# Kernel tuning notes

Measured on AMD Instinct MI355X. Metric: run time of the kernel, lower is better.

## Reference

```python
import jax, jax.numpy as jnp
import numpy as np

B, T, C, H, D, E, K = 4, 1024, 1024, 16, 64, 8, 2
HID = 2 * D  # expert MLP hidden width (assumed 2*head_dim)
NEG = jnp.finfo(jnp.float32).min


def setup_inputs() -> dict:
    key = jax.random.key(0)
    ks = jax.random.split(key, 16)
    s = 0.02
    # rotary tables [max_pos, head_dim]
    inv_freq = 1.0 / (10000.0 ** (jnp.arange(0, D, 2, dtype=jnp.float32) / D))
    freqs = jnp.arange(T, dtype=jnp.float32)[:, None] * inv_freq[None, :]
    emb = jnp.concatenate([freqs, freqs], axis=-1)  # [T, D]
    return {
        "x": jax.random.normal(ks[0], (B, T, C), jnp.float32),
        "position_ids": jnp.sort(jax.random.randint(ks[1], (B, T), 0, T), axis=-1),
        "cos": jnp.cos(emb),
        "sin": jnp.sin(emb),
        "rq": s * jax.random.normal(ks[2], (D, E), jnp.float32),
        "rk": s * jax.random.normal(ks[3], (D, E), jnp.float32),
        "rv": s * jax.random.normal(ks[4], (D, E), jnp.float32),
        "q_w1": s * jax.random.normal(ks[5], (E, D, HID), jnp.float32),
        "q_w2": s * jax.random.normal(ks[6], (E, HID, D), jnp.float32),
        "k_w1": s * jax.random.normal(ks[7], (E, D, HID), jnp.float32),
        "k_w2": s * jax.random.normal(ks[8], (E, HID, D), jnp.float32),
        "v_w1": s * jax.random.normal(ks[9], (E, D, HID), jnp.float32),
        "v_w2": s * jax.random.normal(ks[10], (E, HID, D), jnp.float32),
        "o_w": s * jax.random.normal(ks[11], (C, C), jnp.float32),  # torch Linear weight [out,in]
    }


def _rotate_half(x):
    x1, x2 = x[..., : D // 2], x[..., D // 2:]
    return jnp.concatenate([-x2, x1], axis=-1)


def _moe_head_proj(xh, r_w, w1, w2):
    """Per-head top-k routed expert MLP. xh: [B,T,H,D]."""
    logits = jnp.einsum('bthd,de->bthe', xh, r_w)            # router logits
    vals, idx = jax.lax.top_k(logits, K)                     # [B,T,H,K]
    w = jax.nn.softmax(vals, axis=-1)
    onehot = jax.nn.one_hot(idx, E, dtype=xh.dtype)          # [B,T,H,K,E]
    w_full = jnp.einsum('bthk,bthke->bthe', w, onehot)       # scatter weights to all experts
    h = jax.nn.gelu(jnp.einsum('bthd,edf->bthef', xh, w1))   # all-expert hidden
    out = jnp.einsum('bthe,bthef,efg->bthg', w_full, h, w2)  # masked weighted combine
    return out, logits


def reference(x, position_ids, cos, sin, rq, rk, rv, q_w1, q_w2, k_w1, k_w2, v_w1, v_w2, o_w):
    xh = x.reshape(B, T, H, D)
    q, _ = _moe_head_proj(xh, rq, q_w1, q_w2)
    k, _ = _moe_head_proj(xh, rk, k_w1, k_w2)
    v, _ = _moe_head_proj(xh, rv, v_w1, v_w2)
    q = q.transpose(0, 2, 1, 3)  # [B,H,T,D]
    k = k.transpose(0, 2, 1, 3)
    v = v.transpose(0, 2, 1, 3)
    # RoPE
    c = cos[position_ids][:, None, :, :]  # [B,1,T,D]
    s = sin[position_ids][:, None, :, :]
    q = q * c + _rotate_half(q) * s
    k = k * c + _rotate_half(k) * s
    # causal SDPA
    scores = jnp.einsum('bhqd,bhkd->bhqk', q, k) / jnp.sqrt(jnp.float32(D))
    causal = jnp.tril(jnp.ones((T, T), dtype=bool))
    scores = jnp.where(causal, scores, NEG)
    attn = jax.nn.softmax(scores, axis=-1)
    out = jnp.einsum('bhqk,bhkd->bhqd', attn, v)
    out = out.transpose(0, 2, 1, 3).reshape(B, T, C)
    return out @ o_w.T
```

## Files before the change

### kernel.cpp

```cpp
#include <hip/hip_runtime.h>
#include <math.h>

#define BB 4
#define TT 1024
#define CCH 1024
#define HH 16
#define DD 64
#define EE 8
#define HID 128
#define CAP 8192
#define GEXP 504

typedef unsigned short u16;
typedef unsigned int u32;
typedef short bf16x8 __attribute__((ext_vector_type(8)));
typedef float f32x4 __attribute__((ext_vector_type(4)));

__device__ __forceinline__ u16 f2bf(float f) {
    unsigned int u = __float_as_uint(f);
    unsigned int r = (u + 0x7FFFu + ((u >> 16) & 1u)) >> 16;
    return (u16)r;
}
__device__ __forceinline__ u16 f2bf_f(float f) {
    return (u16)((__float_as_uint(f) + 0x8000u) >> 16);
}
__device__ __forceinline__ u32 pkbf(float lo, float hi) {
    u32 a = __float_as_uint(lo) + 0x8000u;
    u32 b = __float_as_uint(hi) + 0x8000u;
    return __builtin_amdgcn_perm(b, a, 0x07060302u);
}
__device__ __forceinline__ float gelu_fast(float z) {
    float t = z * z;
    float wn = __builtin_fmaf(t, -0.07135481283f, -1.5957691216f);
    float e = __expf(z * wn);
    return __fdividef(z, 1.f + e);
}

#define GLD16(gp, lp) __builtin_amdgcn_global_load_lds( \
    (const __attribute__((address_space(1))) u32*)(gp), \
    (__attribute__((address_space(3))) u32*)(lp), 16, 0, 0)

__global__ __launch_bounds__(256) void prep_kernel(
    const float* __restrict__ x,
    const float* __restrict__ rq, const float* __restrict__ rk, const float* __restrict__ rv,
    unsigned int* __restrict__ counts,
    unsigned int* __restrict__ idxbuf, float2* __restrict__ wtbuf,
    const float* __restrict__ qw1, const float* __restrict__ kw1, const float* __restrict__ vw1,
    const float* __restrict__ qw2, const float* __restrict__ kw2, const float* __restrict__ vw2,
    u16* __restrict__ img1, u16* __restrict__ img2,
    const float* __restrict__ ow, u16* __restrict__ owbf)
{
    const int bi = blockIdx.x;
    const int tid = threadIdx.x;

    if (bi < 192) {
        int t = bi * 256 + tid;
        u16 tmp[8];
        if (t < 24576) {
            int c = t & 7, f = (t >> 3) & 127, e = (t >> 10) & 7, p = t >> 13;
            const float* w1 = ((p == 0) ? qw1 : (p == 1) ? kw1 : vw1) + e * 8192;
            int dbase = 8 * (c ^ (f & 7));
            #pragma unroll
            for (int j = 0; j < 8; ++j) tmp[j] = f2bf(w1[(dbase + j) * 128 + f]);
            uint4 ov;
            ov.x = (u32)tmp[0] | ((u32)tmp[1] << 16);
            ov.y = (u32)tmp[2] | ((u32)tmp[3] << 16);
            ov.z = (u32)tmp[4] | ((u32)tmp[5] << 16);
            ov.w = (u32)tmp[6] | ((u32)tmp[7] << 16);
            ((uint4*)img1)[t] = ov;
        } else {
            int i = t - 24576;
            int c = i & 15, g = (i >> 4) & 63, e = (i >> 10) & 7, p = i >> 13;
            const float* w2 = ((p == 0) ? qw2 : (p == 1) ? kw2 : vw2) + e * 8192;
            int fbase = 8 * (c ^ (g & 15));
            #pragma unroll
            for (int j = 0; j < 8; ++j) tmp[j] = f2bf(w2[(fbase + j) * 64 + g]);
            uint4 ov;
            ov.x = (u32)tmp[0] | ((u32)tmp[1] << 16);
            ov.y = (u32)tmp[2] | ((u32)tmp[3] << 16);
            ov.z = (u32)tmp[4] | ((u32)tmp[5] << 16);
            ov.w = (u32)tmp[6] | ((u32)tmp[7] << 16);
            ((uint4*)img2)[i] = ov;
        }
        return;
    }

    if (bi < 1216) {
        int i = (bi - 192) * 256 + tid;
        float4 v = ((const float4*)ow)[i];
        unsigned int lov = (unsigned int)f2bf(v.x) | ((unsigned int)f2bf(v.y) << 16);
        unsigned int hiv = (unsigned int)f2bf(v.z) | ((unsigned int)f2bf(v.w) << 16);
        ((uint2*)owbf)[i] = make_uint2(lov, hiv);
        return;
    }

    {
        const unsigned int g = (bi - 1216) * 256 + tid;

        __shared__ float rS[3][64][8];
        __shared__ int lcnt[192];
        __shared__ int lbase[192];

        for (int i = tid; i < 1536; i += 256) {
            int p = i >> 9, rem = i & 511;
            const float* rp = (p == 0) ? rq : (p == 1) ? rk : rv;
            rS[p][rem >> 3][rem & 7] = rp[rem];
        }
        if (tid < 192) lcnt[tid] = 0;
        __syncthreads();

        float lg[3][8];
        #pragma unroll
        for (int p = 0; p < 3; ++p)
            #pragma unroll
            for (int e = 0; e < 8; ++e) lg[p][e] = 0.f;

        const float* xr = x + (size_t)g * 64;
        for (int i4 = 0; i4 < 16; ++i4) {
            float4 xv = ((const float4*)xr)[i4];
            float xa[4] = {xv.x, xv.y, xv.z, xv.w};
            #pragma unroll
            for (int m = 0; m < 4; ++m) {
                int d = i4 * 4 + m;
                #pragma unroll
                for (int p = 0; p < 3; ++p) {
                    float4 r0 = *(const float4*)&rS[p][d][0];
                    float4 r1 = *(const float4*)&rS[p][d][4];
                    lg[p][0] += xa[m] * r0.x; lg[p][1] += xa[m] * r0.y;
                    lg[p][2] += xa[m] * r0.z; lg[p][3] += xa[m] * r0.w;
                    lg[p][4] += xa[m] * r1.x; lg[p][5] += xa[m] * r1.y;
                    lg[p][6] += xa[m] * r1.z; lg[p][7] += xa[m] * r1.w;
                }
            }
        }

        int ppe[3]; float2 pw[3]; int slot[3];
        #pragma unroll
        for (int p = 0; p < 3; ++p) {
            int i1 = 0; float v1 = lg[p][0];
            #pragma unroll
            for (int e = 1; e < 8; ++e) { if (lg[p][e] > v1) { v1 = lg[p][e]; i1 = e; } }
            int i2 = -1; float v2 = -3.402823466e38f;
            #pragma unroll
            for (int e = 0; e < 8; ++e) { if (e != i1 && lg[p][e] > v2) { v2 = lg[p][e]; i2 = e; } }
            float z = __expf(v2 - v1);
            float inv = 1.f / (1.f + z);
            float wa = inv, wb = z * inv;
            int lo = min(i1, i2), hi = max(i1, i2);
            float wlo = (i1 < i2) ? wa : wb;
            float whi = (i1 < i2) ? wb : wa;
            int pel = p * 64 + lo * 8 + hi;
            ppe[p] = pel; pw[p] = make_float2(wlo, whi);
            slot[p] = atomicAdd(&lcnt[pel], 1);
        }
        __syncthreads();
        if (tid < 192) {
            int c = lcnt[tid];
            lbase[tid] = c ? (int)atomicAdd(&counts[tid], (unsigned int)c) : 0;
        }
        __syncthreads();
        #pragma unroll
        for (int p = 0; p < 3; ++p) {
            int pos = lbase[ppe[p]] + slot[p];
            if (pos < CAP) {
                idxbuf[ppe[p] * CAP + pos] = g;
                wtbuf[ppe[p] * CAP + pos]  = pw[p];
            }
        }
    }
}

__global__ __launch_bounds__(128) void sched_kernel(
    const unsigned int* __restrict__ counts, unsigned int* __restrict__ blockinfo)
{
    const int tid = threadIdx.x;
    __shared__ int nsub[84];
    __shared__ int extra[84];
    __shared__ int frac[84];
    __shared__ int alloc[84];
    __shared__ int startS[84];
    __shared__ int nnzS, totalS, rem2S;

    if (tid < 84) {
        int p = tid / 28, q = tid - 28 * p, lo = 0;
        while (q >= 7 - lo) { q -= 7 - lo; ++lo; }
        int hi = lo + 1 + q;
        int n = (int)counts[p * 64 + lo * 8 + hi];
        if (n > CAP) n = CAP;
        nsub[tid] = (n + 31) >> 5;
    }
    __syncthreads();
    if (tid == 0) {
        int tot = 0, nz = 0;
        for (int i = 0; i < 84; ++i) { tot += nsub[i]; nz += (nsub[i] > 0); }
        totalS = tot; nnzS = nz;
    }
    __syncthreads();
    const int R = GEXP - nnzS;
    if (tid < 84) {
        if (nsub[tid] > 0) {
            int e = (int)(((long long)nsub[tid] * R) / totalS);
            extra[tid] = e;
            frac[tid] = nsub[tid] * R - e * totalS;
        } else { extra[tid] = 0; frac[tid] = -1; }
    }
    __syncthreads();
    if (tid == 0) {
        int se = 0;
        for (int i = 0; i < 84; ++i) se += extra[i];
        rem2S = GEXP - nnzS - se;
    }
    __syncthreads();
    if (tid < 84) {
        if (nsub[tid] > 0) {
            int rank = 0;
            for (int j = 0; j < 84; ++j)
                if (nsub[j] > 0 && (frac[j] > frac[tid] || (frac[j] == frac[tid] && j < tid))) ++rank;
            alloc[tid] = 1 + extra[tid] + (rank < rem2S ? 1 : 0);
        } else alloc[tid] = 0;
    }
    __syncthreads();
    if (tid == 0) {
        int s = 0;
        for (int i = 0; i < 84; ++i) { startS[i] = s; s += alloc[i]; }
    }
    __syncthreads();
    if (tid < 84) {
        int a = alloc[tid], st = startS[tid];
        for (int c = 0; c < a; ++c)
            blockinfo[st + c] = (unsigned)tid | ((unsigned)c << 8) | ((unsigned)a << 20);
    }
}

__global__ __launch_bounds__(512, 2) void expert_kernel(
    const float* __restrict__ x, const int* __restrict__ pos_ids,
    const float* __restrict__ cosb, const float* __restrict__ sinb,
    const u16* __restrict__ img1, const u16* __restrict__ img2,
    const unsigned int* __restrict__ counts,
    const unsigned int* __restrict__ idxbuf, const float2* __restrict__ wtbuf,
    const unsigned int* __restrict__ blockinfo,
    u16* __restrict__ qb, u16* __restrict__ kb, u16* __restrict__ vb)
{
    const int tid = threadIdx.x;
    const unsigned int info = blockinfo[blockIdx.x];
    const int pe84 = info & 255;
    const int chunk = (info >> 8) & 0xFFF;
    const int nch = info >> 20;
    const int p = pe84 / 28;
    int q28 = pe84 - p * 28;
    int lo = 0;
    while (q28 >= 7 - lo) { q28 -= 7 - lo; ++lo; }
    const int hi = lo + 1 + q28;
    const int pe = p * 64 + lo * 8 + hi;

    int n = (int)counts[pe]; if (n == 0) return; if (n > CAP) n = CAP;

    u16* outp = (p == 0) ? qb : (p == 1) ? kb : vb;
    const unsigned int* il = idxbuf + pe * CAP;
    const float2* wl = wtbuf + pe * CAP;

    __shared__ __align__(16) u16 wsh[32768];

    {
        const u16* a0 = img1 + (p * 8 + lo) * 8192;
        const u16* b0 = img2 + (p * 8 + lo) * 8192;
        const u16* a1 = img1 + (p * 8 + hi) * 8192;
        const u16* b1 = img2 + (p * 8 + hi) * 8192;
        #pragma unroll
        for (int k = 0; k < 2; ++k) {
            int o = (k * 512 + tid) * 8;
            GLD16(a0 + o, wsh + o);
            GLD16(b0 + o, wsh + 8192 + o);
            GLD16(a1 + o, wsh + 16384 + o);
            GLD16(b1 + o, wsh + 24576 + o);
        }
    }
    __syncthreads();

    const int lane = tid & 63, w = tid >> 6, quad = lane >> 4, m16 = lane & 15;
    const int f7 = m16 & 7;
    const int sA = m16 + ((quad & 1) << 5);
    const int sB = sA + 16;
    const int wid = chunk * 8 + w;
    const int WRK = nch * 8;
    const int nsub = (n + 31) >> 5;

    for (int s = wid; s < nsub; s += WRK) {
        const int base = s * 32;
        unsigned int gtok = 0, obase = 0; float wlo_ = 0.f, whi_ = 0.f;
        int posv = 0, valid = 0;
        if (lane < 32) {
            int j = base + lane;
            valid = (j < n);
            int jc = valid ? j : (n - 1);
            gtok = il[jc];
            float2 wv = wl[jc];
            wlo_ = valid ? wv.x : 0.f; whi_ = valid ? wv.y : 0.f;
            unsigned int b_ = gtok >> 14, h_ = gtok & 15, t_ = (gtok >> 4) & 1023;
            obase = ((b_ * 16 + h_) * 1024 + t_) * 64;
            posv = pos_ids[b_ * 1024 + t_];
        }

        float wf00 = __shfl(wlo_, m16, 64);
        float wf10 = __shfl(whi_, m16, 64);
        float wf01 = __shfl(wlo_, 16 + m16, 64);
        float wf11 = __shfl(whi_, 16 + m16, 64);

        bf16x8 Afr[2][2];
        #pragma unroll
        for (int mt2 = 0; mt2 < 2; ++mt2) {
            unsigned int gm = (unsigned int)__shfl((int)gtok, mt2 * 16 + m16, 64);
            const float* xr = x + (size_t)gm * 64 + 8 * quad;
            float4 xa0 = *(const float4*)(xr);
            float4 xa1 = *(const float4*)(xr + 4);
            float4 xb0 = *(const float4*)(xr + 32);
            float4 xb1 = *(const float4*)(xr + 36);
            bf16x8 A0, A1;
            A0[0] = (short)f2bf_f(xa0.x); A0[1] = (short)f2bf_f(xa0.y);
            A0[2] = (short)f2bf_f(xa0.z); A0[3] = (short)f2bf_f(xa0.w);
            A0[4] = (short)f2bf_f(xa1.x); A0[5] = (short)f2bf_f(xa1.y);
            A0[6] = (short)f2bf_f(xa1.z); A0[7] = (short)f2bf_f(xa1.w);
            A1[0] = (short)f2bf_f(xb0.x); A1[1] = (short)f2bf_f(xb0.y);
            A1[2] = (short)f2bf_f(xb0.z); A1[3] = (short)f2bf_f(xb0.w);
            A1[4] = (short)f2bf_f(xb1.x); A1[5] = (short)f2bf_f(xb1.y);
            A1[6] = (short)f2bf_f(xb1.z); A1[7] = (short)f2bf_f(xb1.w);
            Afr[mt2][0] = A0; Afr[mt2][1] = A1;
        }

        f32x4 acc2[2][4];
        #pragma unroll
        for (int mt2 = 0; mt2 < 2; ++mt2)
            #pragma unroll
            for (int nt = 0; nt < 4; ++nt) acc2[mt2][nt] = (f32x4){0.f, 0.f, 0.f, 0.f};

        #pragma unroll 1
        for (int ekk = 0; ekk < 8; ++ekk) {
            const int e = ekk >> 2;
            const int kk = ekk & 3;
            const u16* w1b = wsh + e * 16384;
            const u16* w2b = w1b + 8192;
            const float wt0 = e ? wf10 : wf00;
            const float wt1 = e ? wf11 : wf01;

            f32x4 c[2][2];
            #pragma unroll
            for (int ntl = 0; ntl < 2; ++ntl) {
                const int f = 16 * (2 * kk + ntl) + m16;
                const u16* w1f = w1b + f * 64;
                bf16x8 wa = *(const bf16x8*)(w1f + (((quad    ) ^ f7) << 3));
                bf16x8 wb = *(const bf16x8*)(w1f + (((quad + 4) ^ f7) << 3));
                #pragma unroll
                for (int mt2 = 0; mt2 < 2; ++mt2) {
                    f32x4 t = (f32x4){0.f, 0.f, 0.f, 0.f};
                    t = __builtin_amdgcn_mfma_f32_16x16x32_bf16(wa, Afr[mt2][0], t, 0, 0, 0);
                    c[ntl][mt2] = __builtin_amdgcn_mfma_f32_16x16x32_bf16(wb, Afr[mt2][1], t, 0, 0, 0);
                }
            }
            const int c2base = (((4 * kk + quad) ^ m16) << 3);
            #pragma unroll
            for (int mt2 = 0; mt2 < 2; ++mt2) {
                const float wt = mt2 ? wt1 : wt0;
                u32 pl0, ph0, pl1, ph1;
                {
                    float g0 = wt * gelu_fast(c[0][mt2][0]);
                    float g1 = wt * gelu_fast(c[0][mt2][1]);
                    float g2 = wt * gelu_fast(c[0][mt2][2]);
                    float g3 = wt * gelu_fast(c[0][mt2][3]);
                    pl0 = pkbf(g0, g1); ph0 = pkbf(g2, g3);
                    g0 = wt * gelu_fast(c[1][mt2][0]);
                    g1 = wt * gelu_fast(c[1][mt2][1]);
                    g2 = wt * gelu_fast(c[1][mt2][2]);
                    g3 = wt * gelu_fast(c[1][mt2][3]);
                    pl1 = pkbf(g0, g1); ph1 = pkbf(g2, g3);
                }
                u32 q0l = (u32)__shfl((int)pl0, sA, 64);
                u32 q1l = (u32)__shfl((int)pl1, sA, 64);
                u32 q0h = (u32)__shfl((int)ph0, sA, 64);
                u32 q1h = (u32)__shfl((int)ph1, sA, 64);
                u32 r0l = (u32)__shfl((int)pl0, sB, 64);
                u32 r1l = (u32)__shfl((int)pl1, sB, 64);
                u32 r0h = (u32)__shfl((int)ph0, sB, 64);
                u32 r1h = (u32)__shfl((int)ph1, sB, 64);
                const bool hisel = (quad & 2);
                union { u32 u[4]; bf16x8 v; } a2;
                a2.u[0] = hisel ? q1l : q0l;
                a2.u[1] = hisel ? q1h : q0h;
                a2.u[2] = hisel ? r1l : r0l;
                a2.u[3] = hisel ? r1h : r0h;
                #pragma unroll
                for (int nt2 = 0; nt2 < 4; ++nt2) {
                    const u16* w2f = w2b + (16 * nt2 + m16) * 128 + c2base;
                    bf16x8 b2 = *(const bf16x8*)w2f;
                    acc2[mt2][nt2] = __builtin_amdgcn_mfma_f32_16x16x32_bf16(a2.v, b2, acc2[mt2][nt2], 0, 0, 0);
                }
            }
        }

        #pragma unroll
        for (int mt2 = 0; mt2 < 2; ++mt2) {
            #pragma unroll
            for (int r = 0; r < 4; ++r) {
                int tk = mt2 * 16 + 4 * quad + r;
                int   pos_r = __shfl(posv, tk, 64);
                unsigned int ob = (unsigned int)__shfl((int)obase, tk, 64);
                int   val_r = __shfl(valid, tk, 64);
                if (p < 2) {
                    #pragma unroll
                    for (int ntp = 0; ntp < 2; ++ntp) {
                        int d = 16 * ntp + m16;
                        float v1 = acc2[mt2][ntp][r];
                        float v2 = acc2[mt2][ntp + 2][r];
                        float cd = cosb[pos_r * 64 + d];
                        float sd = sinb[pos_r * 64 + d];
                        if (val_r) {
                            outp[ob + d]      = f2bf(v1 * cd - v2 * sd);
                            outp[ob + d + 32] = f2bf(v2 * cd + v1 * sd);
                        }
                    }
                } else {
                    #pragma unroll
                    for (int nt = 0; nt < 4; ++nt) {
                        float v = acc2[mt2][nt][r];
                        if (val_r) outp[ob + 16 * nt + m16] = f2bf(v);
                    }
                }
            }
        }
    }
}

__global__ __launch_bounds__(256) void attn_kernel(
    const u16* __restrict__ qbp, const u16* __restrict__ kbp,
    const u16* __restrict__ vbp, u16* __restrict__ ao)
{
    const int tid = threadIdx.x;
    const int i8 = blockIdx.x & 7;
    const int plane_i = blockIdx.x >> 3;
    const int h = plane_i & 15, b = plane_i >> 4;
    const size_t plane = (size_t)plane_i * 1024 * 64;
    const u16* qp = qbp + plane;
    const u16* kp = kbp + plane;
    const u16* vp = vbp + plane;

    const int w = tid >> 6, lane = tid & 63, quad = lane >> 4, m16 = lane & 15;
    const int row = tid >> 2, seg = tid & 3;
    const int kjv = tid & 63, dgv = tid >> 6;

    __shared__ u16 Ks[64][72];
    __shared__ u16 Vt[64][72];
    __shared__ u16 Ps[4][16][72];

    #pragma unroll 1
    for (int half = 0; half < 2; ++half) {
        const int qt = half ? (15 - i8) : i8;
        const int q0 = qt * 64;

        const u16* qrow = &qp[(size_t)(q0 + 16 * w + m16) * 64 + 8 * quad];
        bf16x8 aq0 = *(const bf16x8*)(qrow);
        bf16x8 aq1 = *(const bf16x8*)(qrow + 32);

        uint4 kr0, kr1; ushort4 vr0, vr1, vr2, vr3;
        {
            const uint4* src = (const uint4*)&kp[(size_t)row * 64 + seg * 16];
            kr0 = src[0]; kr1 = src[1];
            const u16* vb2 = &vp[(size_t)kjv * 64 + dgv * 4];
            vr0 = *(const ushort4*)(vb2);
            vr1 = *(const ushort4*)(vb2 + 16);
            vr2 = *(const ushort4*)(vb2 + 32);
            vr3 = *(const ushort4*)(vb2 + 48);
        }

        float m_r[4], l_r[4];
        #pragma unroll
        for (int i = 0; i < 4; ++i) { m_r[i] = -1e30f; l_r[i] = 0.f; }
        f32x4 oacc[4];
        #pragma unroll
        for (int i = 0; i < 4; ++i) oacc[i] = (f32x4){0.f, 0.f, 0.f, 0.f};

        for (int kt = 0; kt <= qt; ++kt) {
            __syncthreads();
            {
                uint4* dst = (uint4*)&Ks[row][seg * 16];
                dst[0] = kr0; dst[1] = kr1;
                int d0 = dgv * 4;
                Vt[d0 + 0][kjv] = vr0.x; Vt[d0 + 1][kjv] = vr0.y;
                Vt[d0 + 2][kjv] = vr0.z; Vt[d0 + 3][kjv] = vr0.w;
                Vt[d0 + 16][kjv] = vr1.x; Vt[d0 + 17][kjv] = vr1.y;
                Vt[d0 + 18][kjv] = vr1.z; Vt[d0 + 19][kjv] = vr1.w;
                Vt[d0 + 32][kjv] = vr2.x; Vt[d0 + 33][kjv] = vr2.y;
                Vt[d0 + 34][kjv] = vr2.z; Vt[d0 + 35][kjv] = vr2.w;
                Vt[d0 + 48][kjv] = vr3.x; Vt[d0 + 49][kjv] = vr3.y;
                Vt[d0 + 50][kjv] = vr3.z; Vt[d0 + 51][kjv] = vr3.w;
            }
            __syncthreads();
            if (kt < qt) {
                const int k0n = (kt + 1) * 64;
                const uint4* src = (const uint4*)&kp[(size_t)(k0n + row) * 64 + seg * 16];
                kr0 = src[0]; kr1 = src[1];
                const u16* vb2 = &vp[(size_t)(k0n + kjv) * 64 + dgv * 4];
                vr0 = *(const ushort4*)(vb2);
                vr1 = *(const ushort4*)(vb2 + 16);
                vr2 = *(const ushort4*)(vb2 + 32);
                vr3 = *(const ushort4*)(vb2 + 48);
            }

            f32x4 sv[4];
            #pragma unroll
            for (int ct = 0; ct < 4; ++ct) {
                bf16x8 bk0 = *(const bf16x8*)&Ks[16 * ct + m16][8 * quad];
                bf16x8 bk1 = *(const bf16x8*)&Ks[16 * ct + m16][32 + 8 * quad];
                f32x4 acc = (f32x4){0.f, 0.f, 0.f, 0.f};
                acc = __builtin_amdgcn_mfma_f32_16x16x32_bf16(aq0, bk0, acc, 0, 0, 0);
                acc = __builtin_amdgcn_mfma_f32_16x16x32_bf16(aq1, bk1, acc, 0, 0, 0);
                sv[ct] = acc;
            }

            float s[4][4];
            const bool diag = (kt == qt);
            #pragma unroll
            for (int ct = 0; ct < 4; ++ct)
                #pragma unroll
                for (int reg = 0; reg < 4; ++reg) {
                    float v = sv[ct][reg] * 0.125f;
                    if (diag) {
                        int col = 16 * ct + m16;
                        int rw = 16 * w + 4 * quad + reg;
                        if (col > rw) v = -1e30f;
                    }
                    s[ct][reg] = v;
                }

            float nm[4], al[4];
            #pragma unroll
            for (int reg = 0; reg < 4; ++reg) {
                float rm = fmaxf(fmaxf(s[0][reg], s[1][reg]), fmaxf(s[2][reg], s[3][reg]));
                #pragma unroll
                for (int off = 1; off < 16; off <<= 1) rm = fmaxf(rm, __shfl_xor(rm, off, 16));
                float mn = fmaxf(m_r[reg], rm);
                nm[reg] = mn;
                al[reg] = __expf(m_r[reg] - mn);
            }
            #pragma unroll
            for (int reg = 0; reg < 4; ++reg) {
                float sum = 0.f;
                #pragma unroll
                for (int ct = 0; ct < 4; ++ct) {
                    float pv = __expf(s[ct][reg] - nm[reg]);
                    s[ct][reg] = pv;
                    sum += pv;
                }
                #pragma unroll
                for (int off = 1; off < 16; off <<= 1) sum += __shfl_xor(sum, off, 16);
                l_r[reg] = l_r[reg] * al[reg] + sum;
                m_r[reg] = nm[reg];
            }

            #pragma unroll
            for (int ct = 0; ct < 4; ++ct)
                #pragma unroll
                for (int reg = 0; reg < 4; ++reg)
                    Ps[w][4 * quad + reg][16 * ct + m16] = f2bf(s[ct][reg]);

            #pragma unroll
            for (int dt = 0; dt < 4; ++dt)
                #pragma unroll
                for (int reg = 0; reg < 4; ++reg) oacc[dt][reg] *= al[reg];

            bf16x8 ap0 = *(const bf16x8*)&Ps[w][m16][8 * quad];
            bf16x8 ap1 = *(const bf16x8*)&Ps[w][m16][32 + 8 * quad];
            #pragma unroll
            for (int dt = 0; dt < 4; ++dt) {
                bf16x8 bv0 = *(const bf16x8*)&Vt[16 * dt + m16][8 * quad];
                bf16x8 bv1 = *(const bf16x8*)&Vt[16 * dt + m16][32 + 8 * quad];
                oacc[dt] = __builtin_amdgcn_mfma_f32_16x16x32_bf16(ap0, bv0, oacc[dt], 0, 0, 0);
                oacc[dt] = __builtin_amdgcn_mfma_f32_16x16x32_bf16(ap1, bv1, oacc[dt], 0, 0, 0);
            }
        }

        #pragma unroll
        for (int reg = 0; reg < 4; ++reg) {
            float linv = 1.f / l_r[reg];
            int rw = q0 + 16 * w + 4 * quad + reg;
            size_t base = ((size_t)(b * 1024) + rw) * 1024 + h * 64;
            #pragma unroll
            for (int dt = 0; dt < 4; ++dt)
                ao[base + 16 * dt + m16] = f2bf(oacc[dt][reg] * linv);
        }
    }
}

__global__ __launch_bounds__(256) void oproj_kernel(
    const u16* __restrict__ A, const u16* __restrict__ Bw,
    float* __restrict__ out)
{
    const int tid = threadIdx.x;
    const int bn = blockIdx.x & 7;
    const int bm = blockIdx.x >> 3;
    const int m0 = bm * 128, n0 = bn * 128;
    const int w = tid >> 6, lane = tid & 63, quad = lane >> 4, m16 = lane & 15;
    const int wm = (w >> 1) * 64, wn = (w & 1) * 64;

    __shared__ u16 As[128][32];
    __shared__ u16 Bs[128][32];

    f32x4 acc[4][4];
    #pragma unroll
    for (int mt = 0; mt < 4; ++mt)
        #pragma unroll
        for (int nt = 0; nt < 4; ++nt) acc[mt][nt] = (f32x4){0.f, 0.f, 0.f, 0.f};

    for (int k0 = 0; k0 < 1024; k0 += 32) {
        __syncthreads();
        {
            int rw = tid >> 1, sg = (tid & 1) * 16;
            const uint4* srcA = (const uint4*)&A[(size_t)(m0 + rw) * 1024 + k0 + sg];
            uint4 a0 = srcA[0], a1 = srcA[1];
            uint4* dstA = (uint4*)&As[rw][sg];
            dstA[0] = a0; dstA[1] = a1;
            const uint4* srcB = (const uint4*)&Bw[(size_t)(n0 + rw) * 1024 + k0 + sg];
            uint4 b0 = srcB[0], b1 = srcB[1];
            uint4* dstB = (uint4*)&Bs[rw][sg];
            dstB[0] = b0; dstB[1] = b1;
        }
        __syncthreads();
        bf16x8 af[4], bf_[4];
        #pragma unroll
        for (int mt = 0; mt < 4; ++mt) af[mt] = *(const bf16x8*)&As[wm + 16 * mt + m16][8 * quad];
        #pragma unroll
        for (int nt = 0; nt < 4; ++nt) bf_[nt] = *(const bf16x8*)&Bs[wn + 16 * nt + m16][8 * quad];
        #pragma unroll
        for (int mt = 0; mt < 4; ++mt)
            #pragma unroll
            for (int nt = 0; nt < 4; ++nt)
                acc[mt][nt] = __builtin_amdgcn_mfma_f32_16x16x32_bf16(af[mt], bf_[nt], acc[mt][nt], 0, 0, 0);
    }
    #pragma unroll
    for (int mt = 0; mt < 4; ++mt)
        #pragma unroll
        for (int nt = 0; nt < 4; ++nt)
            #pragma unroll
            for (int reg = 0; reg < 4; ++reg)
                out[(size_t)(m0 + wm + 16 * mt + 4 * quad + reg) * 1024 + n0 + wn + 16 * nt + m16] =
                    acc[mt][nt][reg];
}

extern "C" void kernel_launch(void* const* d_in, const int* in_sizes, int n_in,
                              void* d_out, int out_size, void* d_ws, size_t ws_size,
                              hipStream_t stream) {
    (void)in_sizes; (void)n_in; (void)out_size; (void)ws_size;
    const float* x    = (const float*)d_in[0];
    const int*   pid  = (const int*)  d_in[1];
    const float* cosb = (const float*)d_in[2];
    const float* sinb = (const float*)d_in[3];
    const float* rq   = (const float*)d_in[4];
    const float* rk   = (const float*)d_in[5];
    const float* rv   = (const float*)d_in[6];
    const float* qw1  = (const float*)d_in[7];
    const float* qw2  = (const float*)d_in[8];
    const float* kw1  = (const float*)d_in[9];
    const float* kw2  = (const float*)d_in[10];
    const float* vw1  = (const float*)d_in[11];
    const float* vw2  = (const float*)d_in[12];
    const float* ow   = (const float*)d_in[13];
    float* out = (float*)d_out;

    const size_t MB = 1u << 20;
    char* wsb = (char*)d_ws;
    u16* qb   = (u16*)(wsb + 0 * MB);
    u16* kb   = (u16*)(wsb + 8 * MB);
    u16* vb   = (u16*)(wsb + 16 * MB);
    u16* aobf = (u16*)(wsb + 24 * MB);
    u16* owbf = (u16*)(wsb + 32 * MB);
    unsigned int* idxbuf = (unsigned int*)(wsb + 34 * MB);
    float2*       wtbuf  = (float2*)(wsb + 41 * MB);
    unsigned int* counts = (unsigned int*)(wsb + 54 * MB);
    unsigned int* blockinfo = (unsigned int*)(wsb + 54 * MB + 4096);
    u16* w1img = (u16*)(wsb + 56 * MB);
    u16* w2img = (u16*)(wsb + 57 * MB);

    hipMemsetAsync(counts, 0, 1024, stream);

    hipLaunchKernelGGL(prep_kernel, dim3(1472), dim3(256), 0, stream,
                       x, rq, rk, rv, counts, idxbuf, wtbuf,
                       qw1, kw1, vw1, qw2, kw2, vw2, w1img, w2img,
                       ow, owbf);
    hipLaunchKernelGGL(sched_kernel, dim3(1), dim3(128), 0, stream,
                       counts, blockinfo);
    hipLaunchKernelGGL(expert_kernel, dim3(GEXP), dim3(512), 0, stream,
                       x, pid, cosb, sinb, w1img, w2img,
                       counts, idxbuf, wtbuf, blockinfo, qb, kb, vb);
    hipLaunchKernelGGL(attn_kernel, dim3(512), dim3(256), 0, stream,
                       qb, kb, vb, aobf);
    hipLaunchKernelGGL(oproj_kernel, dim3(256), dim3(256), 0, stream,
                       aobf, owbf, out);
}
```

Measured before the change: 241.9 us.

## Feed GELU output straight into 16x16x16 MFMA and vectorize RoPE stores

Reorders the W2 bf16 image into 4-element swizzled groups so the first GEMM's accumulator fragments can act directly as the B operand of mfma 16x16x16 bf16 for the second GEMM. This removes the eight cross-lane shuffles and selects per tile that rebuilt the A operand for 16x16x32 MFMA. With W2 as the A operand, the output is transposed so each lane holds four consecutive d values, allowing float4 cos/sin loads and 8-byte packed bf16 stores instead of scalar ones. The trade-off is twice as many smaller MFMA instructions and more register-held W2 fragments.

```diff
diff --git a/kernel.cpp b/kernel.cpp
--- a/kernel.cpp
+++ b/kernel.cpp
@@ -14,6 +14,7 @@
 typedef unsigned short u16;
 typedef unsigned int u32;
 typedef short bf16x8 __attribute__((ext_vector_type(8)));
+typedef short bf16x4 __attribute__((ext_vector_type(4)));
 typedef float f32x4 __attribute__((ext_vector_type(4)));
 
 __device__ __forceinline__ u16 f2bf(float f) {
@@ -55,11 +56,11 @@
 
     if (bi < 192) {
         int t = bi * 256 + tid;
-        u16 tmp[8];
         if (t < 24576) {
             int c = t & 7, f = (t >> 3) & 127, e = (t >> 10) & 7, p = t >> 13;
             const float* w1 = ((p == 0) ? qw1 : (p == 1) ? kw1 : vw1) + e * 8192;
             int dbase = 8 * (c ^ (f & 7));
+            u16 tmp[8];
             #pragma unroll
             for (int j = 0; j < 8; ++j) tmp[j] = f2bf(w1[(dbase + j) * 128 + f]);
             uint4 ov;
@@ -70,17 +71,23 @@
             ((uint4*)img1)[t] = ov;
         } else {
             int i = t - 24576;
-            int c = i & 15, g = (i >> 4) & 63, e = (i >> 10) & 7, p = i >> 13;
+            int m = i & 15, g = (i >> 4) & 63, e = (i >> 10) & 7, p = i >> 13;
             const float* w2 = ((p == 0) ? qw2 : (p == 1) ? kw2 : vw2) + e * 8192;
-            int fbase = 8 * (c ^ (g & 15));
-            #pragma unroll
-            for (int j = 0; j < 8; ++j) tmp[j] = f2bf(w2[(fbase + j) * 64 + g]);
-            uint4 ov;
-            ov.x = (u32)tmp[0] | ((u32)tmp[1] << 16);
-            ov.y = (u32)tmp[2] | ((u32)tmp[3] << 16);
-            ov.z = (u32)tmp[4] | ((u32)tmp[5] << 16);
-            ov.w = (u32)tmp[6] | ((u32)tmp[7] << 16);
-            ((uint4*)img2)[i] = ov;
+            u16* dstrow = img2 + (p * 8 + e) * 8192 + g * 128;
+            #pragma unroll
+            for (int u = 0; u < 2; ++u) {
+                int gg = 2 * m + u;
+                int fbase = 16 * (gg >> 2) + 4 * (gg & 3);
+                int pos = gg ^ (g & 31);
+                u16 a0 = f2bf(w2[(fbase + 0) * 64 + g]);
+                u16 a1 = f2bf(w2[(fbase + 1) * 64 + g]);
+                u16 a2 = f2bf(w2[(fbase + 2) * 64 + g]);
+                u16 a3 = f2bf(w2[(fbase + 3) * 64 + g]);
+                uint2 ov;
+                ov.x = (u32)a0 | ((u32)a1 << 16);
+                ov.y = (u32)a2 | ((u32)a3 << 16);
+                *(uint2*)(dstrow + pos * 4) = ov;
+            }
         }
         return;
     }
@@ -279,8 +286,6 @@
 
     const int lane = tid & 63, w = tid >> 6, quad = lane >> 4, m16 = lane & 15;
     const int f7 = m16 & 7;
-    const int sA = m16 + ((quad & 1) << 5);
-    const int sB = sA + 16;
     const int wid = chunk * 8 + w;
     const int WRK = nch * 8;
     const int nsub = (n + 31) >> 5;
@@ -356,72 +361,78 @@
                     c[ntl][mt2] = __builtin_amdgcn_mfma_f32_16x16x32_bf16(wb, Afr[mt2][1], t, 0, 0, 0);
                 }
             }
-            const int c2base = (((4 * kk + quad) ^ m16) << 3);
+
+            bf16x4 w2f[2][4];
+            #pragma unroll
+            for (int ntl = 0; ntl < 2; ++ntl) {
+                const int gg = 4 * (2 * kk + ntl) + quad;
+                #pragma unroll
+                for (int nt2 = 0; nt2 < 4; ++nt2) {
+                    const int g = 16 * nt2 + m16;
+                    const int pos = gg ^ (g & 31);
+                    w2f[ntl][nt2] = *(const bf16x4*)(w2b + g * 128 + pos * 4);
+                }
+            }
+
             #pragma unroll
             for (int mt2 = 0; mt2 < 2; ++mt2) {
                 const float wt = mt2 ? wt1 : wt0;
-                u32 pl0, ph0, pl1, ph1;
-                {
-                    float g0 = wt * gelu_fast(c[0][mt2][0]);
-                    float g1 = wt * gelu_fast(c[0][mt2][1]);
-                    float g2 = wt * gelu_fast(c[0][mt2][2]);
-                    float g3 = wt * gelu_fast(c[0][mt2][3]);
-                    pl0 = pkbf(g0, g1); ph0 = pkbf(g2, g3);
-                    g0 = wt * gelu_fast(c[1][mt2][0]);
-                    g1 = wt * gelu_fast(c[1][mt2][1]);
-                    g2 = wt * gelu_fast(c[1][mt2][2]);
-                    g3 = wt * gelu_fast(c[1][mt2][3]);
-                    pl1 = pkbf(g0, g1); ph1 = pkbf(g2, g3);
+                #pragma unroll
+                for (int ntl = 0; ntl < 2; ++ntl) {
+                    float g0 = wt * gelu_fast(c[ntl][mt2][0]);
+                    float g1 = wt * gelu_fast(c[ntl][mt2][1]);
+                    float g2 = wt * gelu_fast(c[ntl][mt2][2]);
+                    float g3 = wt * gelu_fast(c[ntl][mt2][3]);
+                    union { u32 u[2]; bf16x4 v; } bf_;
+                    bf_.u[0] = pkbf(g0, g1);
+                    bf_.u[1] = pkbf(g2, g3);
+                    #pragma unroll
+                    for (int nt2 = 0; nt2 < 4; ++nt2)
+                        acc2[mt2][nt2] = __builtin_amdgcn_mfma_f32_16x16x16bf16_1k(
+                            w2f[ntl][nt2], bf_.v, acc2[mt2][nt2], 0, 0, 0);
                 }
-                u32 q0l = (u32)__shfl((int)pl0, sA, 64);
-                u32 q1l = (u32)__shfl((int)pl1, sA, 64);
-                u32 q0h = (u32)__shfl((int)ph0, sA, 64);
-                u32 q1h = (u32)__shfl((int)ph1, sA, 64);
-                u32 r0l = (u32)__shfl((int)pl0, sB, 64);
-                u32 r1l = (u32)__shfl((int)pl1, sB, 64);
-                u32 r0h = (u32)__shfl((int)ph0, sB, 64);
-                u32 r1h = (u32)__shfl((int)ph1, sB, 64);
-                const bool hisel = (quad & 2);
-                union { u32 u[4]; bf16x8 v; } a2;
-                a2.u[0] = hisel ? q1l : q0l;
-                a2.u[1] = hisel ? q1h : q0h;
-                a2.u[2] = hisel ? r1l : r0l;
-                a2.u[3] = hisel ? r1h : r0h;
-                #pragma unroll
-                for (int nt2 = 0; nt2 < 4; ++nt2) {
-                    const u16* w2f = w2b + (16 * nt2 + m16) * 128 + c2base;
-                    bf16x8 b2 = *(const bf16x8*)w2f;
-                    acc2[mt2][nt2] = __builtin_amdgcn_mfma_f32_16x16x32_bf16(a2.v, b2, acc2[mt2][nt2], 0, 0, 0);
-                }
             }
         }
 
         #pragma unroll
         for (int mt2 = 0; mt2 < 2; ++mt2) {
-            #pragma unroll
-            for (int r = 0; r < 4; ++r) {
-                int tk = mt2 * 16 + 4 * quad + r;
-                int   pos_r = __shfl(posv, tk, 64);
-                unsigned int ob = (unsigned int)__shfl((int)obase, tk, 64);
-                int   val_r = __shfl(valid, tk, 64);
-                if (p < 2) {
+            const int tk = mt2 * 16 + m16;
+            int   pos_r = __shfl(posv, tk, 64);
+            unsigned int ob = (unsigned int)__shfl((int)obase, tk, 64);
+            int   val_r = __shfl(valid, tk, 64);
+            if (p < 2) {
+                #pragma unroll
+                for (int ntp = 0; ntp < 2; ++ntp) {
+                    const int d0 = 16 * ntp + 4 * quad;
+                    float4 cv = *(const float4*)&cosb[pos_r * 64 + d0];
+                    float4 sv = *(const float4*)&sinb[pos_r * 64 + d0];
+                    float o1[4], o2[4];
                     #pragma unroll
-                    for (int ntp = 0; ntp < 2; ++ntp) {
-                        int d = 16 * ntp + m16;
+                    for (int r = 0; r < 4; ++r) {
                         float v1 = acc2[mt2][ntp][r];
                         float v2 = acc2[mt2][ntp + 2][r];
-                        float cd = cosb[pos_r * 64 + d];
-                        float sd = sinb[pos_r * 64 + d];
-                        if (val_r) {
-                            outp[ob + d]      = f2bf(v1 * cd - v2 * sd);
-                            outp[ob + d + 32] = f2bf(v2 * cd + v1 * sd);
-                        }
+                        float cd = (&cv.x)[r], sd = (&sv.x)[r];
+                        o1[r] = v1 * cd - v2 * sd;
+                        o2[r] = v2 * cd + v1 * sd;
                     }
-                } else {
+                    if (val_r) {
+                        uint2 s1, s2;
+                        s1.x = (u32)f2bf(o1[0]) | ((u32)f2bf(o1[1]) << 16);
+                        s1.y = (u32)f2bf(o1[2]) | ((u32)f2bf(o1[3]) << 16);
+                        s2.x = (u32)f2bf(o2[0]) | ((u32)f2bf(o2[1]) << 16);
+                        s2.y = (u32)f2bf(o2[2]) | ((u32)f2bf(o2[3]) << 16);
+                        *(uint2*)&outp[ob + d0]      = s1;
+                        *(uint2*)&outp[ob + d0 + 32] = s2;
+                    }
+                }
+            } else {
+                if (val_r) {
                     #pragma unroll
-                    for (int nt = 0; nt < 4; ++nt) {
-                        float v = acc2[mt2][nt][r];
-                        if (val_r) outp[ob + 16 * nt + m16] = f2bf(v);
+                    for (int nt2 = 0; nt2 < 4; ++nt2) {
+                        uint2 s1;
+                        s1.x = (u32)f2bf(acc2[mt2][nt2][0]) | ((u32)f2bf(acc2[mt2][nt2][1]) << 16);
+                        s1.y = (u32)f2bf(acc2[mt2][nt2][2]) | ((u32)f2bf(acc2[mt2][nt2][3]) << 16);
+                        *(uint2*)&outp[ob + 16 * nt2 + 4 * quad] = s1;
                     }
                 }
             }
```

After: 237.8 us. About the same (-1.7%).
